# Optimization experiments

Hardware: AMD Instinct MI355X
Metric: run time of the kernel (lower is better)

Reference implementation:

```python
import jax, jax.numpy as jnp
import numpy as np

DIM = 1024
HEADS = 8
HEAD_DIM = DIM // HEADS
TAU = HEAD_DIM ** 0.5
BS, SEQ = 1, 2048


def setup_inputs() -> dict:
    key = jax.random.key(0)
    kq, kk, kv, kb = jax.random.split(key, 4)
    q = jax.random.normal(kq, (BS, SEQ, DIM), jnp.float32)
    k = jax.random.normal(kk, (BS, SEQ, DIM), jnp.float32)
    v = jax.random.normal(kv, (BS, SEQ, DIM), jnp.float32)
    Wi_w = jnp.zeros((HEADS, 3 * DIM), jnp.float32)
    Wi_b = 0.1 * jax.random.normal(kb, (HEADS,), jnp.float32)
    Wf_w = jnp.zeros((HEADS, 3 * DIM), jnp.float32)
    Wf_b = jnp.linspace(3.0, 6.0, HEADS, dtype=jnp.float32)  # equidistant_bias_init(3, 6)
    gn_w = jnp.ones((DIM,), jnp.float32)
    gn_b = jnp.zeros((DIM,), jnp.float32)
    return {"q": q, "k": k, "v": v, "Wi_w": Wi_w, "Wi_b": Wi_b,
            "Wf_w": Wf_w, "Wf_b": Wf_b, "gn_w": gn_w, "gn_b": gn_b}


def reference(q, k, v, Wi_w, Wi_b, Wf_w, Wf_b, gn_w, gn_b):
    bs, seq, dim = q.shape
    gate_in = jnp.concatenate([q, k, v], axis=-1)                    # [b, s, 3d]
    itilde = jnp.einsum('bsd,hd->bhs', gate_in, Wi_w) + Wi_b[None, :, None]
    ftilde = jnp.einsum('bsd,hd->bhs', gate_in, Wf_w) + Wf_b[None, :, None]

    # Decay matrix: F_act[i,j] = sum_{t=j+1..i} logsigmoid(ftilde_t), lower-tri else -inf
    csum = jnp.cumsum(jax.nn.log_sigmoid(ftilde), axis=-1)           # [b, h, s]
    Fmat = csum[..., :, None] - csum[..., None, :]                   # [b, h, s, s]
    mask = jnp.tril(jnp.ones((seq, seq), dtype=bool))
    F_act = jnp.where(mask, Fmat, -jnp.inf)

    Dtilde = F_act + itilde[..., None, :]                            # add input gate along j
    max_d = jnp.max(Dtilde, axis=-1, keepdims=True)
    D = jnp.exp(Dtilde - max_d)                                      # stabilized decay weights

    qh = q.reshape(bs, seq, HEADS, HEAD_DIM).transpose(0, 2, 1, 3)
    kh = k.reshape(bs, seq, HEADS, HEAD_DIM).transpose(0, 2, 1, 3)
    vh = v.reshape(bs, seq, HEADS, HEAD_DIM).transpose(0, 2, 1, 3)

    Ctilde = jnp.einsum('bhid,bhjd->bhij', qh, kh) * D / TAU
    maxit = jnp.maximum(jnp.abs(jnp.sum(Ctilde, axis=-1, keepdims=True)), jnp.exp(-max_d))
    Htilde = jnp.einsum('bhij,bhjd->bhid', Ctilde, vh) / (maxit + 1e-6)

    # GroupNorm(HEADS groups) over dim, applied per token
    x = Htilde.transpose(0, 2, 1, 3).reshape(bs * seq, HEADS, HEAD_DIM)
    mean = jnp.mean(x, axis=-1, keepdims=True)
    var = jnp.var(x, axis=-1, keepdims=True)
    xn = (x - mean) / jnp.sqrt(var + 1e-5)
    out = xn.reshape(bs * seq, DIM) * gn_w + gn_b
    return out.reshape(bs, seq, DIM)
```

## Files before the change

kernel.cpp:

```cpp
#include <hip/hip_runtime.h>
#include <math.h>

#define SEQ 2048
#define NH 8
#define HD 128
#define DIMF 1024
#define LOG2E 1.4426950408889634f
#define INVTAU 0.08838834764831845f

typedef __attribute__((ext_vector_type(8))) short bf16x8;
typedef __attribute__((ext_vector_type(8))) unsigned short us8;
typedef __attribute__((ext_vector_type(4))) float f32x4;
typedef __attribute__((ext_vector_type(16))) float f32x16;

__device__ float g_itacc[NH*SEQ];
__device__ float g_ftacc[NH*SEQ];
__device__ float g_aL[NH*SEQ];
__device__ float g_cmL[NH*SEQ];
__device__ float g_en[NH*SEQ];
__device__ unsigned short g_Qb[NH*SEQ*HD];
__device__ unsigned short g_Kb[NH*SEQ*HD];
__device__ unsigned short g_Vb[NH*SEQ*HD];
__device__ unsigned short g_Vt[NH*HD*SEQ];
__device__ unsigned short g_Wb[16*3072];
__device__ float g_Opart[640*64*128];
__device__ float g_Spart[640*64];

__device__ __forceinline__ unsigned short f2bf(float x) {
  unsigned u = __float_as_uint(x);
  u += 0x7fffu + ((u >> 16) & 1u);
  return (unsigned short)(u >> 16);
}

__device__ __forceinline__ unsigned packbf(float lo, float hi) {
  return (unsigned)f2bf(lo) | ((unsigned)f2bf(hi) << 16);
}

__global__ __launch_bounds__(256) void convert_kernel(const float* __restrict__ q,
                                                      const float* __restrict__ k,
                                                      const float* __restrict__ v,
                                                      const float* __restrict__ Wi,
                                                      const float* __restrict__ Wf) {
  const int bid = blockIdx.x;
  if (bid < 6144) {
    const int s = bid & 2047;
    const int t = bid >> 11;
    const float* src = (t == 0) ? q : (t == 1) ? k : v;
    unsigned short* dst = (t == 0) ? g_Qb : (t == 1) ? g_Kb : g_Vb;
    const int c = threadIdx.x * 4;
    const float4 f = *(const float4*)(src + s*DIMF + c);
    const int h = c >> 7, d = c & 127;
    ushort4 u;
    u.x = f2bf(f.x); u.y = f2bf(f.y); u.z = f2bf(f.z); u.w = f2bf(f.w);
    *(ushort4*)(dst + (h*SEQ + s)*HD + d) = u;
  } else {
    const int gid = (bid - 6144) * 256 + threadIdx.x;
    const int e4 = gid * 4;
    const int p = e4 / 3072;
    const int c = e4 % 3072;
    const float* src = (p < 8) ? (Wi + p*3072 + c) : (Wf + (p-8)*3072 + c);
    const float4 f = *(const float4*)src;
    ushort4 u;
    u.x = f2bf(f.x); u.y = f2bf(f.y); u.z = f2bf(f.z); u.w = f2bf(f.w);
    *(ushort4*)(g_Wb + p*3072 + c) = u;
  }
}

__global__ __launch_bounds__(256) void vtrans_kernel() {
  __shared__ __align__(16) unsigned short Ts[64*72];
  const int h  = blockIdx.x;
  const int s0 = blockIdx.y * 64;
  const int d0 = blockIdx.z * 64;
  const int t = threadIdx.x;
  {
    const int sr = t >> 2;
    const int c  = (t & 3) * 16;
    const unsigned short* src = g_Vb + (h*SEQ + s0 + sr)*HD + d0 + c;
    *(us8*)&Ts[sr*72 + c]     = *(const us8*)&src[0];
    *(us8*)&Ts[sr*72 + c + 8] = *(const us8*)&src[8];
  }
  __syncthreads();
  {
    const int w = t >> 6, l = t & 63;
    unsigned short outv[16];
    #pragma unroll
    for (int j = 0; j < 16; ++j) outv[j] = Ts[(w*16 + j)*72 + l];
    unsigned short* dst = g_Vt + (h*HD + d0 + l)*SEQ + s0 + w*16;
    *(us8*)&dst[0] = *(us8*)&outv[0];
    *(us8*)&dst[8] = *(us8*)&outv[8];
  }
}

__global__ __launch_bounds__(256) void gates_kernel() {
  __shared__ f32x4 red[4][64];
  const int tid = threadIdx.x;
  const int wave = tid >> 6, lane = tid & 63;
  const int q4 = lane >> 4, l16 = lane & 15;
  const int s0 = blockIdx.x * 16;
  f32x4 acc = {0.f, 0.f, 0.f, 0.f};
  #pragma unroll 8
  for (int ks = wave*24; ks < wave*24 + 24; ++ks) {
    const int k0 = ks*32 + q4*8;
    const int tsel = k0 >> 10;
    const int rem = k0 & 1023;
    const int hh = rem >> 7, dd = rem & 127;
    const unsigned short* base = (tsel == 0) ? g_Qb : (tsel == 1) ? g_Kb : g_Vb;
    const bf16x8 a = *(const bf16x8*)&base[(hh*SEQ + s0 + l16)*HD + dd];
    const bf16x8 b = *(const bf16x8*)&g_Wb[l16*3072 + k0];
    acc = __builtin_amdgcn_mfma_f32_16x16x32_bf16(a, b, acc, 0, 0, 0);
  }
  red[wave][lane] = acc;
  __syncthreads();
  if (wave == 0) {
    f32x4 s = red[0][lane];
    #pragma unroll
    for (int w = 1; w < 4; ++w) s += red[w][lane];
    #pragma unroll
    for (int r = 0; r < 4; ++r) {
      const int sg = s0 + 4*q4 + r;
      if (l16 < 8) g_itacc[l16*SEQ + sg] = s[r];
      else         g_ftacc[(l16-8)*SEQ + sg] = s[r];
    }
  }
}

__global__ __launch_bounds__(256) void scan_kernel(const float* __restrict__ Wi_b,
                                                   const float* __restrict__ Wf_b) {
  __shared__ float Wsum[4];
  __shared__ float Wmax[4];
  const int h = blockIdx.x;
  const int t = threadIdx.x;
  const int wave = t >> 6, lane = t & 63;
  const float ib = Wi_b[h];
  const float fb = Wf_b[h];
  const int base = h*SEQ + t*8;

  float it[8], ft[8];
  *(float4*)&it[0] = *(const float4*)&g_itacc[base];
  *(float4*)&it[4] = *(const float4*)&g_itacc[base+4];
  *(float4*)&ft[0] = *(const float4*)&g_ftacc[base];
  *(float4*)&ft[4] = *(const float4*)&g_ftacc[base+4];

  float cs[8];
  float run = 0.f;
  #pragma unroll
  for (int j = 0; j < 8; ++j) {
    const float f = ft[j] + fb;
    const float ls = fminf(f, 0.f) - log1pf(expf(-fabsf(f)));
    run += ls;
    cs[j] = run;
  }
  float x = run;
  #pragma unroll
  for (int off = 1; off < 64; off <<= 1) {
    const float tv = __shfl_up(x, off, 64);
    if (lane >= off) x += tv;
  }
  const float wexcl = x - run;
  if (lane == 63) Wsum[wave] = x;
  __syncthreads();
  float boff = 0.f;
  #pragma unroll
  for (int w = 0; w < 4; ++w) if (w < wave) boff += Wsum[w];
  const float cbase = boff + wexcl;

  float a[8], am[8], csum[8];
  float m = -__builtin_inff();
  #pragma unroll
  for (int j = 0; j < 8; ++j) {
    csum[j] = cbase + cs[j];
    a[j] = (it[j] + ib) - csum[j];
    m = fmaxf(m, a[j]);
    am[j] = m;
  }
  float y = m;
  #pragma unroll
  for (int off = 1; off < 64; off <<= 1) {
    const float tv = __shfl_up(y, off, 64);
    if (lane >= off) y = fmaxf(y, tv);
  }
  float e = __shfl_up(y, 1, 64);
  if (lane == 0) e = -__builtin_inff();
  if (lane == 63) Wmax[wave] = y;
  __syncthreads();
  float bmax = -__builtin_inff();
  #pragma unroll
  for (int w = 0; w < 4; ++w) if (w < wave) bmax = fmaxf(bmax, Wmax[w]);
  const float pre = fmaxf(bmax, e);

  float oa[8], ocm[8], oen[8];
  #pragma unroll
  for (int j = 0; j < 8; ++j) {
    const float cm = fmaxf(pre, am[j]);
    oa[j]  = a[j] * LOG2E;
    ocm[j] = cm * LOG2E;
    oen[j] = expf(-(csum[j] + cm));
  }
  *(float4*)&g_aL[base]    = *(float4*)&oa[0];
  *(float4*)&g_aL[base+4]  = *(float4*)&oa[4];
  *(float4*)&g_cmL[base]   = *(float4*)&ocm[0];
  *(float4*)&g_cmL[base+4] = *(float4*)&ocm[4];
  *(float4*)&g_en[base]    = *(float4*)&oen[0];
  *(float4*)&g_en[base+4]  = *(float4*)&oen[4];
}

__global__ __launch_bounds__(256, 2) void attn1_kernel() {
  __shared__ float Osum[2][32][128];
  __shared__ float Sred[64][2];

  const int y = blockIdx.x;
  const int h = blockIdx.y;
  int g, s0g;
  if      (y < 8)  { g = 0; s0g = 0;  }
  else if (y < 24) { g = 1; s0g = 8;  }
  else if (y < 48) { g = 2; s0g = 24; }
  else             { g = 3; s0g = 48; }
  const int rel = y - s0g;
  const int iT  = 8*g + rel/(g+1);
  const int ch  = rel - (rel/(g+1))*(g+1);
  const int slot = h*80 + y;
  const int i0 = iT*64;
  const int jt0 = ch*8;
  const int jt1 = (jt0 + 8 < iT + 1) ? (jt0 + 8) : (iT + 1);

  const int tid  = threadIdx.x;
  const int wave = tid >> 6;
  const int lane = tid & 63;
  const int l31  = lane & 31;
  const int hi   = lane >> 5;
  const int wr   = wave >> 1;
  const int wc   = wave & 1;

  bf16x8 qf[8];
  {
    const unsigned short* Qg = g_Qb + (h*SEQ + i0 + 32*wr + l31)*HD + hi*8;
    #pragma unroll
    for (int ks = 0; ks < 8; ++ks) qf[ks] = *(const bf16x8*)&Qg[ks*16];
  }
  const float cm = g_cmL[h*SEQ + i0 + 32*wr + l31];
  const int   ig = i0 + 32*wr + l31;

  f32x16 acc[4];
  #pragma unroll
  for (int td = 0; td < 4; ++td)
    #pragma unroll
    for (int e = 0; e < 16; ++e) acc[td][e] = 0.f;
  float rs_sum = 0.f;

  const unsigned short* Kg  = g_Kb + (h*SEQ + 32*wc + l31)*HD + hi*8;
  const unsigned short* Vg  = g_Vt + (h*HD + l31)*SEQ + 32*wc + hi*8;
  const float*          aLg = g_aL + h*SEQ + 32*wc + 4*hi;

  for (int jt = jt0; jt < jt1; ++jt) {
    const int j0 = jt*64;
    bf16x8 kf[8];
    #pragma unroll
    for (int ks = 0; ks < 8; ++ks) kf[ks] = *(const bf16x8*)&Kg[j0*HD + ks*16];
    float4 aLq[4];
    #pragma unroll
    for (int rq = 0; rq < 4; ++rq) aLq[rq] = *(const float4*)&aLg[j0 + 8*rq];

    f32x16 a0, a1;
    #pragma unroll
    for (int e = 0; e < 16; ++e) { a0[e] = 0.f; a1[e] = 0.f; }
    #pragma unroll
    for (int ks = 0; ks < 8; ks += 2) {
      a0 = __builtin_amdgcn_mfma_f32_32x32x16_bf16(kf[ks],   qf[ks],   a0, 0, 0, 0);
      a1 = __builtin_amdgcn_mfma_f32_32x32x16_bf16(kf[ks+1], qf[ks+1], a1, 0, 0, 0);
    }

    const bool diag = (jt == iT);
    const int jbase = j0 + 32*wc + 4*hi;

    #pragma unroll
    for (int ph = 0; ph < 2; ++ph) {
      float pv[8];
      #pragma unroll
      for (int rr = 0; rr < 8; ++rr) {
        const int r  = 8*ph + rr;
        const int rq = r >> 2;
        const float aL = ((const float*)&aLq[rq])[r & 3];
        float p = (a0[r] + a1[r]) * (exp2f(aL - cm) * INVTAU);
        const int jg = jbase + 8*rq + (r & 3);
        if (diag && jg > ig) p = 0.f;
        rs_sum += p;
        pv[rr] = p;
      }
      const unsigned w0 = packbf(pv[0], pv[1]);
      const unsigned w1 = packbf(pv[2], pv[3]);
      const unsigned w2 = packbf(pv[4], pv[5]);
      const unsigned w3 = packbf(pv[6], pv[7]);
      const auto s0 = __builtin_amdgcn_permlane32_swap(w0, w2, false, false);
      const auto s1 = __builtin_amdgcn_permlane32_swap(w1, w3, false, false);
      union { unsigned u[4]; bf16x8 v; } fr;
      fr.u[0] = s0[0]; fr.u[1] = s1[0]; fr.u[2] = s0[1]; fr.u[3] = s1[1];
      #pragma unroll
      for (int td = 0; td < 4; ++td) {
        const bf16x8 vb = *(const bf16x8*)&Vg[(32*td)*SEQ + j0 + 16*ph];
        acc[td] = __builtin_amdgcn_mfma_f32_32x32x16_bf16(fr.v, vb, acc[td], 0, 0, 0);
      }
    }
  }

  rs_sum += __shfl_xor(rs_sum, 32, 64);
  if (hi == 0) Sred[32*wr + l31][wc] = rs_sum;

  if (wc == 0) {
    #pragma unroll
    for (int td = 0; td < 4; ++td)
      #pragma unroll
      for (int r = 0; r < 16; ++r) {
        const int row = (r & 3) + 8*(r >> 2) + 4*hi;
        Osum[wr][row][32*td + l31] = acc[td][r];
      }
  }
  __syncthreads();
  if (wc == 1) {
    float* Ob = g_Opart + slot*(64*128);
    #pragma unroll
    for (int td = 0; td < 4; ++td)
      #pragma unroll
      for (int r = 0; r < 16; ++r) {
        const int row = (r & 3) + 8*(r >> 2) + 4*hi;
        Ob[(32*wr + row)*128 + 32*td + l31] = acc[td][r] + Osum[wr][row][32*td + l31];
      }
  }
  if (tid < 64) g_Spart[slot*64 + tid] = Sred[tid][0] + Sred[tid][1];
}

__global__ __launch_bounds__(256) void reduce_kernel(const float* __restrict__ gnw,
                                                     const float* __restrict__ gnb,
                                                     float* __restrict__ out) {
  const int h  = blockIdx.x;
  const int iT = blockIdx.y;
  const int t  = threadIdx.x;
  const int r  = t >> 2;
  const int qd = t & 3;
  const int qq = iT >> 3;
  const int nch = qq + 1;
  const int slot0 = h*80 + iT + 4*qq*(qq-1) + qq*(iT & 7);

  float acc[32];
  #pragma unroll
  for (int e = 0; e < 32; ++e) acc[e] = 0.f;
  float S = 0.f;
  for (int c = 0; c < nch; ++c) {
    const float* Ob = g_Opart + (slot0 + c)*(64*128) + r*128 + qd*32;
    #pragma unroll
    for (int kk = 0; kk < 8; ++kk) {
      const float4 f = *(const float4*)&Ob[kk*4];
      acc[kk*4+0] += f.x; acc[kk*4+1] += f.y; acc[kk*4+2] += f.z; acc[kk*4+3] += f.w;
    }
    S += g_Spart[(slot0 + c)*64 + r];
  }

  const float en = g_en[h*SEQ + iT*64 + r];
  const float sc = 1.f / (fmaxf(fabsf(S), en) + 1e-6f);
  float s1 = 0.f, s2 = 0.f;
  #pragma unroll
  for (int e = 0; e < 32; ++e) {
    const float xv = acc[e] * sc;
    acc[e] = xv;
    s1 += xv;
    s2 += xv * xv;
  }
  s1 += __shfl_xor(s1, 1, 4); s2 += __shfl_xor(s2, 1, 4);
  s1 += __shfl_xor(s1, 2, 4); s2 += __shfl_xor(s2, 2, 4);
  const float mean = s1 * (1.f/128.f);
  const float var  = s2 * (1.f/128.f) - mean*mean;
  const float rstd = rsqrtf(var + 1e-5f);

  const float* gw = gnw + h*HD + qd*32;
  const float* gb = gnb + h*HD + qd*32;
  float* op = out + (iT*64 + r)*DIMF + h*HD + qd*32;
  #pragma unroll
  for (int kk = 0; kk < 8; ++kk) {
    const float4 w4 = *(const float4*)&gw[kk*4];
    const float4 b4 = *(const float4*)&gb[kk*4];
    float4 o;
    o.x = (acc[kk*4+0] - mean) * rstd * w4.x + b4.x;
    o.y = (acc[kk*4+1] - mean) * rstd * w4.y + b4.y;
    o.z = (acc[kk*4+2] - mean) * rstd * w4.z + b4.z;
    o.w = (acc[kk*4+3] - mean) * rstd * w4.w + b4.w;
    *(float4*)&op[kk*4] = o;
  }
}

extern "C" void kernel_launch(void* const* d_in, const int* in_sizes, int n_in,
                              void* d_out, int out_size, void* d_ws, size_t ws_size,
                              hipStream_t stream) {
  (void)in_sizes; (void)n_in; (void)out_size; (void)d_ws; (void)ws_size;
  const float* q    = (const float*)d_in[0];
  const float* k    = (const float*)d_in[1];
  const float* v    = (const float*)d_in[2];
  const float* Wi_w = (const float*)d_in[3];
  const float* Wi_b = (const float*)d_in[4];
  const float* Wf_w = (const float*)d_in[5];
  const float* Wf_b = (const float*)d_in[6];
  const float* gnw  = (const float*)d_in[7];
  const float* gnb  = (const float*)d_in[8];
  float* out = (float*)d_out;

  convert_kernel<<<dim3(6192), 256, 0, stream>>>(q, k, v, Wi_w, Wf_w);
  vtrans_kernel<<<dim3(NH, SEQ/64, HD/64), 256, 0, stream>>>();
  gates_kernel<<<dim3(128), 256, 0, stream>>>();
  scan_kernel<<<dim3(NH), 256, 0, stream>>>(Wi_b, Wf_b);
  attn1_kernel<<<dim3(80, NH), 256, 0, stream>>>();
  reduce_kernel<<<dim3(NH, SEQ/64), 256, 0, stream>>>(gnw, gnb, out);
}
```

Baseline: 172.9 us.

## Stage K/V tiles in LDS via direct global-to-LDS loads and split work finer

The attention kernel now loads each K and transposed-V 64-row tile into swizzled shared memory with global_load_lds, where all four waves share it. Before, each wave fetched its own fragments straight from global memory. The key-dimension chunks are halved from 8 tiles to 4, so each head gets 144 blocks instead of 80. The grid is reordered so heads vary fastest, and occupancy is raised to 3 blocks per CU. The cost is two barriers per tile with no double buffering, more partial sums for the reduce kernel to combine, and Osum reusing the K/V shared buffer.

```diff
diff --git a/kernel.cpp b/kernel.cpp
--- a/kernel.cpp
+++ b/kernel.cpp
@@ -7,6 +7,7 @@
 #define DIMF 1024
 #define LOG2E 1.4426950408889634f
 #define INVTAU 0.08838834764831845f
+#define NSLOT 144
 
 typedef __attribute__((ext_vector_type(8))) short bf16x8;
 typedef __attribute__((ext_vector_type(8))) unsigned short us8;
@@ -23,8 +24,8 @@
 __device__ unsigned short g_Vb[NH*SEQ*HD];
 __device__ unsigned short g_Vt[NH*HD*SEQ];
 __device__ unsigned short g_Wb[16*3072];
-__device__ float g_Opart[640*64*128];
-__device__ float g_Spart[640*64];
+__device__ float g_Opart[NH*NSLOT*64*128];
+__device__ float g_Spart[NH*NSLOT*64];
 
 __device__ __forceinline__ unsigned short f2bf(float x) {
   unsigned u = __float_as_uint(x);
@@ -34,6 +35,12 @@
 
 __device__ __forceinline__ unsigned packbf(float lo, float hi) {
   return (unsigned)f2bf(lo) | ((unsigned)f2bf(hi) << 16);
+}
+
+__device__ __forceinline__ void gload16(const unsigned short* g, unsigned short* l) {
+  __builtin_amdgcn_global_load_lds(
+      (const __attribute__((address_space(1))) unsigned int*)g,
+      (__attribute__((address_space(3))) unsigned int*)l, 16, 0, 0);
 }
 
 __global__ __launch_bounds__(256) void convert_kernel(const float* __restrict__ q,
@@ -204,24 +211,24 @@
   *(float4*)&g_en[base+4]  = *(float4*)&oen[4];
 }
 
-__global__ __launch_bounds__(256, 2) void attn1_kernel() {
-  __shared__ float Osum[2][32][128];
-  __shared__ float Sred[64][2];
-
-  const int y = blockIdx.x;
-  const int h = blockIdx.y;
-  int g, s0g;
-  if      (y < 8)  { g = 0; s0g = 0;  }
-  else if (y < 24) { g = 1; s0g = 8;  }
-  else if (y < 48) { g = 2; s0g = 24; }
-  else             { g = 3; s0g = 48; }
+__global__ __launch_bounds__(256, 3) void attn1_kernel() {
+  __shared__ __align__(16) unsigned char smem[33280];
+  unsigned short* Ks = (unsigned short*)smem;
+  unsigned short* Vt = (unsigned short*)(smem + 16384);
+  float (*Osum)[32][128] = (float (*)[32][128])smem;
+  float (*Sred)[2] = (float (*)[2])(smem + 32768);
+
+  const int h = blockIdx.x;
+  const int y = blockIdx.y;
+  int q = 0, s0g = 0;
+  while (y >= s0g + 4*(q+1)) { s0g += 4*(q+1); ++q; }
   const int rel = y - s0g;
-  const int iT  = 8*g + rel/(g+1);
-  const int ch  = rel - (rel/(g+1))*(g+1);
-  const int slot = h*80 + y;
+  const int iT  = 4*q + rel/(q+1);
+  const int ch  = rel - (rel/(q+1))*(q+1);
+  const int slot = h*NSLOT + y;
   const int i0 = iT*64;
-  const int jt0 = ch*8;
-  const int jt1 = (jt0 + 8 < iT + 1) ? (jt0 + 8) : (iT + 1);
+  const int jt0 = ch*4;
+  const int jt1 = (jt0 + 4 < iT + 1) ? (jt0 + 4) : (iT + 1);
 
   const int tid  = threadIdx.x;
   const int wave = tid >> 6;
@@ -230,6 +237,7 @@
   const int hi   = lane >> 5;
   const int wr   = wave >> 1;
   const int wc   = wave & 1;
+  const int wbase = __builtin_amdgcn_readfirstlane(wave);
 
   bf16x8 qf[8];
   {
@@ -247,26 +255,49 @@
     for (int e = 0; e < 16; ++e) acc[td][e] = 0.f;
   float rs_sum = 0.f;
 
-  const unsigned short* Kg  = g_Kb + (h*SEQ + 32*wc + l31)*HD + hi*8;
-  const unsigned short* Vg  = g_Vt + (h*HD + l31)*SEQ + 32*wc + hi*8;
+  const unsigned short* Kgh = g_Kb + h*SEQ*HD;
+  const unsigned short* Vgh = g_Vt + h*HD*SEQ;
   const float*          aLg = g_aL + h*SEQ + 32*wc + 4*hi;
+
+  int pK[4], pV[4];
+  #pragma unroll
+  for (int gi = 0; gi < 4; ++gi) {
+    const int s  = (wave*4 + gi)*64 + lane;
+    const int rK = s >> 4;
+    const int cK = (s & 15) ^ (rK & 15);
+    pK[gi] = rK*HD + cK*8;
+    const int dV = s >> 3;
+    const int cV = (s & 7) ^ (dV & 7);
+    pV[gi] = dV*SEQ + cV*8;
+  }
+
+  const int rI = 32*wc + l31;
+  const unsigned short* KsRow = &Ks[rI*128];
+  const int swK = rI & 15;
 
   for (int jt = jt0; jt < jt1; ++jt) {
     const int j0 = jt*64;
-    bf16x8 kf[8];
-    #pragma unroll
-    for (int ks = 0; ks < 8; ++ks) kf[ks] = *(const bf16x8*)&Kg[j0*HD + ks*16];
+    __syncthreads();
+    #pragma unroll
+    for (int gi = 0; gi < 4; ++gi) {
+      gload16(Kgh + j0*HD + pK[gi], &Ks[(wbase*4 + gi)*512]);
+      gload16(Vgh + j0     + pV[gi], &Vt[(wbase*4 + gi)*512]);
+    }
     float4 aLq[4];
     #pragma unroll
     for (int rq = 0; rq < 4; ++rq) aLq[rq] = *(const float4*)&aLg[j0 + 8*rq];
+    asm volatile("s_waitcnt vmcnt(0)" ::: "memory");
+    __syncthreads();
 
     f32x16 a0, a1;
     #pragma unroll
     for (int e = 0; e < 16; ++e) { a0[e] = 0.f; a1[e] = 0.f; }
     #pragma unroll
     for (int ks = 0; ks < 8; ks += 2) {
-      a0 = __builtin_amdgcn_mfma_f32_32x32x16_bf16(kf[ks],   qf[ks],   a0, 0, 0, 0);
-      a1 = __builtin_amdgcn_mfma_f32_32x32x16_bf16(kf[ks+1], qf[ks+1], a1, 0, 0, 0);
+      const bf16x8 k0v = *(const bf16x8*)&KsRow[((ks*2 + hi)     ^ swK)*8];
+      const bf16x8 k1v = *(const bf16x8*)&KsRow[(((ks+1)*2 + hi) ^ swK)*8];
+      a0 = __builtin_amdgcn_mfma_f32_32x32x16_bf16(k0v, qf[ks],   a0, 0, 0, 0);
+      a1 = __builtin_amdgcn_mfma_f32_32x32x16_bf16(k1v, qf[ks+1], a1, 0, 0, 0);
     }
 
     const bool diag = (jt == iT);
@@ -296,7 +327,8 @@
       fr.u[0] = s0[0]; fr.u[1] = s1[0]; fr.u[2] = s0[1]; fr.u[3] = s1[1];
       #pragma unroll
       for (int td = 0; td < 4; ++td) {
-        const bf16x8 vb = *(const bf16x8*)&Vg[(32*td)*SEQ + j0 + 16*ph];
+        const int d = 32*td + l31;
+        const bf16x8 vb = *(const bf16x8*)&Vt[d*64 + (((4*wc + 2*ph + hi) ^ (d & 7))*8)];
         acc[td] = __builtin_amdgcn_mfma_f32_32x32x16_bf16(fr.v, vb, acc[td], 0, 0, 0);
       }
     }
@@ -304,6 +336,7 @@
 
   rs_sum += __shfl_xor(rs_sum, 32, 64);
   if (hi == 0) Sred[32*wr + l31][wc] = rs_sum;
+  __syncthreads();
 
   if (wc == 0) {
     #pragma unroll
@@ -336,9 +369,9 @@
   const int t  = threadIdx.x;
   const int r  = t >> 2;
   const int qd = t & 3;
-  const int qq = iT >> 3;
+  const int qq = iT >> 2;
   const int nch = qq + 1;
-  const int slot0 = h*80 + iT + 4*qq*(qq-1) + qq*(iT & 7);
+  const int slot0 = h*NSLOT + 2*qq*(qq+1) + (iT & 3)*(qq + 1);
 
   float acc[32];
   #pragma unroll
@@ -405,6 +438,6 @@
   vtrans_kernel<<<dim3(NH, SEQ/64, HD/64), 256, 0, stream>>>();
   gates_kernel<<<dim3(128), 256, 0, stream>>>();
   scan_kernel<<<dim3(NH), 256, 0, stream>>>(Wi_b, Wf_b);
-  attn1_kernel<<<dim3(80, NH), 256, 0, stream>>>();
+  attn1_kernel<<<dim3(NH, NSLOT), 256, 0, stream>>>();
   reduce_kernel<<<dim3(NH, SEQ/64), 256, 0, stream>>>(gnw, gnb, out);
 }
```

After: 168.5 us. 1.03x faster.

## Fuse attention and GroupNorm reduction with paired causal tiles per block

Applied to the files above, without the earlier changes.

Replaces the split-K attention kernel and its separate reduce kernel with one kernel. Each block pairs a short and a long 32-row query tile (y and 63-y) so the causal work is balanced, shares the K/V loads between both tiles, and double-buffers K/V in registers. The partial sums are reduced in shared memory and the GroupNorm epilogue runs in the same kernel. This removes the partial-output round trip through global memory and one launch. In exchange the grid is smaller (256 blocks at one block per CU) and register pressure is high.

```diff
diff --git a/kernel.cpp b/kernel.cpp
--- a/kernel.cpp
+++ b/kernel.cpp
@@ -23,8 +23,6 @@
 __device__ unsigned short g_Vb[NH*SEQ*HD];
 __device__ unsigned short g_Vt[NH*HD*SEQ];
 __device__ unsigned short g_Wb[16*3072];
-__device__ float g_Opart[640*64*128];
-__device__ float g_Spart[640*64];
 
 __device__ __forceinline__ unsigned short f2bf(float x) {
   unsigned u = __float_as_uint(x);
@@ -204,186 +202,198 @@
   *(float4*)&g_en[base+4]  = *(float4*)&oen[4];
 }
 
-__global__ __launch_bounds__(256, 2) void attn1_kernel() {
-  __shared__ float Osum[2][32][128];
-  __shared__ float Sred[64][2];
-
-  const int y = blockIdx.x;
-  const int h = blockIdx.y;
-  int g, s0g;
-  if      (y < 8)  { g = 0; s0g = 0;  }
-  else if (y < 24) { g = 1; s0g = 8;  }
-  else if (y < 48) { g = 2; s0g = 24; }
-  else             { g = 3; s0g = 48; }
-  const int rel = y - s0g;
-  const int iT  = 8*g + rel/(g+1);
-  const int ch  = rel - (rel/(g+1))*(g+1);
-  const int slot = h*80 + y;
-  const int i0 = iT*64;
-  const int jt0 = ch*8;
-  const int jt1 = (jt0 + 8 < iT + 1) ? (jt0 + 8) : (iT + 1);
+__global__ __launch_bounds__(256, 1) void attn_kernel(const float* __restrict__ gnw,
+                                                      const float* __restrict__ gnb,
+                                                      float* __restrict__ out) {
+  __shared__ float Osum[2][32][132];
+  __shared__ float Sred[4][32];
+
+  const int h = blockIdx.x;
+  const int y = blockIdx.y;
+  const int tS = y, tB = 63 - y;
+  const int iS0 = 32*tS, iB0 = 32*tB;
+  const int iSmax = iS0 + 31, iBmax = iB0 + 31;
+  const int nvB = tB/4 + 1;
 
   const int tid  = threadIdx.x;
-  const int wave = tid >> 6;
+  const int w    = tid >> 6;
   const int lane = tid & 63;
   const int l31  = lane & 31;
   const int hi   = lane >> 5;
-  const int wr   = wave >> 1;
-  const int wc   = wave & 1;
-
-  bf16x8 qf[8];
+
+  const unsigned short* Kgh = g_Kb + (h*SEQ + l31)*HD + hi*8;
+  const unsigned short* Vgh = g_Vt + (h*HD + l31)*SEQ + hi*8;
+  const float*          aLh = g_aL + h*SEQ + 4*hi;
+
+  bf16x8 qfS[8], qfB[8];
   {
-    const unsigned short* Qg = g_Qb + (h*SEQ + i0 + 32*wr + l31)*HD + hi*8;
-    #pragma unroll
-    for (int ks = 0; ks < 8; ++ks) qf[ks] = *(const bf16x8*)&Qg[ks*16];
-  }
-  const float cm = g_cmL[h*SEQ + i0 + 32*wr + l31];
-  const int   ig = i0 + 32*wr + l31;
-
-  f32x16 acc[4];
+    const unsigned short* QS = g_Qb + (h*SEQ + iS0 + l31)*HD + hi*8;
+    const unsigned short* QB = g_Qb + (h*SEQ + iB0 + l31)*HD + hi*8;
+    #pragma unroll
+    for (int ks = 0; ks < 8; ++ks) {
+      qfS[ks] = *(const bf16x8*)&QS[ks*16];
+      qfB[ks] = *(const bf16x8*)&QB[ks*16];
+    }
+  }
+  const float cmS = g_cmL[h*SEQ + iS0 + l31];
+  const float cmB = g_cmL[h*SEQ + iB0 + l31];
+  const int   igS = iS0 + l31, igB = iB0 + l31;
+
+  f32x16 accS[4], accB[4];
   #pragma unroll
   for (int td = 0; td < 4; ++td)
     #pragma unroll
-    for (int e = 0; e < 16; ++e) acc[td][e] = 0.f;
-  float rs_sum = 0.f;
-
-  const unsigned short* Kg  = g_Kb + (h*SEQ + 32*wc + l31)*HD + hi*8;
-  const unsigned short* Vg  = g_Vt + (h*HD + l31)*SEQ + 32*wc + hi*8;
-  const float*          aLg = g_aL + h*SEQ + 32*wc + 4*hi;
-
-  for (int jt = jt0; jt < jt1; ++jt) {
-    const int j0 = jt*64;
-    bf16x8 kf[8];
-    #pragma unroll
-    for (int ks = 0; ks < 8; ++ks) kf[ks] = *(const bf16x8*)&Kg[j0*HD + ks*16];
-    float4 aLq[4];
-    #pragma unroll
-    for (int rq = 0; rq < 4; ++rq) aLq[rq] = *(const float4*)&aLg[j0 + 8*rq];
-
-    f32x16 a0, a1;
-    #pragma unroll
-    for (int e = 0; e < 16; ++e) { a0[e] = 0.f; a1[e] = 0.f; }
+    for (int e = 0; e < 16; ++e) { accS[td][e] = 0.f; accB[td][e] = 0.f; }
+  float rsS = 0.f, rsB = 0.f;
+
+  bf16x8 Ka[8], Va[8], Kb[8], Vb[8];
+
+  auto LOAD = [&](bf16x8 (&K)[8], bf16x8 (&V)[8], int jc) {
+    const int jw = jc*128 + 32*w;
+    #pragma unroll
+    for (int ks = 0; ks < 8; ++ks)
+      K[ks] = *(const bf16x8*)&Kgh[jw*HD + ks*16];
+    #pragma unroll
+    for (int td = 0; td < 4; ++td)
+      #pragma unroll
+      for (int ph = 0; ph < 2; ++ph)
+        V[td*2 + ph] = *(const bf16x8*)&Vgh[(32*td)*SEQ + jw + 16*ph];
+  };
+
+  auto TILE = [&](int jw, const bf16x8 (&K)[8], const bf16x8 (&V)[8],
+                  const float4 (&aLq)[4], const bf16x8 (&qf)[8],
+                  float cm, int ig, int i0t, f32x16 (&acc)[4], float& rsum) {
+    f32x16 s0a, s1a;
+    #pragma unroll
+    for (int e = 0; e < 16; ++e) { s0a[e] = 0.f; s1a[e] = 0.f; }
     #pragma unroll
     for (int ks = 0; ks < 8; ks += 2) {
-      a0 = __builtin_amdgcn_mfma_f32_32x32x16_bf16(kf[ks],   qf[ks],   a0, 0, 0, 0);
-      a1 = __builtin_amdgcn_mfma_f32_32x32x16_bf16(kf[ks+1], qf[ks+1], a1, 0, 0, 0);
-    }
-
-    const bool diag = (jt == iT);
-    const int jbase = j0 + 32*wc + 4*hi;
-
+      s0a = __builtin_amdgcn_mfma_f32_32x32x16_bf16(K[ks],   qf[ks],   s0a, 0, 0, 0);
+      s1a = __builtin_amdgcn_mfma_f32_32x32x16_bf16(K[ks+1], qf[ks+1], s1a, 0, 0, 0);
+    }
+    const bool needMask = (jw + 31 > i0t);
     #pragma unroll
     for (int ph = 0; ph < 2; ++ph) {
       float pv[8];
-      #pragma unroll
-      for (int rr = 0; rr < 8; ++rr) {
-        const int r  = 8*ph + rr;
-        const int rq = r >> 2;
-        const float aL = ((const float*)&aLq[rq])[r & 3];
-        float p = (a0[r] + a1[r]) * (exp2f(aL - cm) * INVTAU);
-        const int jg = jbase + 8*rq + (r & 3);
-        if (diag && jg > ig) p = 0.f;
-        rs_sum += p;
-        pv[rr] = p;
+      if (needMask) {
+        #pragma unroll
+        for (int rr = 0; rr < 8; ++rr) {
+          const int r  = 8*ph + rr;
+          const int rq = r >> 2;
+          const float aL = ((const float*)&aLq[rq])[r & 3];
+          float p = (s0a[r] + s1a[r]) * (exp2f(aL - cm) * INVTAU);
+          const int jg = jw + 8*rq + 4*hi + (r & 3);
+          if (jg > ig) p = 0.f;
+          rsum += p;
+          pv[rr] = p;
+        }
+      } else {
+        #pragma unroll
+        for (int rr = 0; rr < 8; ++rr) {
+          const int r  = 8*ph + rr;
+          const int rq = r >> 2;
+          const float aL = ((const float*)&aLq[rq])[r & 3];
+          const float p = (s0a[r] + s1a[r]) * (exp2f(aL - cm) * INVTAU);
+          rsum += p;
+          pv[rr] = p;
+        }
       }
       const unsigned w0 = packbf(pv[0], pv[1]);
       const unsigned w1 = packbf(pv[2], pv[3]);
       const unsigned w2 = packbf(pv[4], pv[5]);
       const unsigned w3 = packbf(pv[6], pv[7]);
-      const auto s0 = __builtin_amdgcn_permlane32_swap(w0, w2, false, false);
-      const auto s1 = __builtin_amdgcn_permlane32_swap(w1, w3, false, false);
+      const auto p0 = __builtin_amdgcn_permlane32_swap(w0, w2, false, false);
+      const auto p1 = __builtin_amdgcn_permlane32_swap(w1, w3, false, false);
       union { unsigned u[4]; bf16x8 v; } fr;
-      fr.u[0] = s0[0]; fr.u[1] = s1[0]; fr.u[2] = s0[1]; fr.u[3] = s1[1];
+      fr.u[0] = p0[0]; fr.u[1] = p1[0]; fr.u[2] = p0[1]; fr.u[3] = p1[1];
       #pragma unroll
-      for (int td = 0; td < 4; ++td) {
-        const bf16x8 vb = *(const bf16x8*)&Vg[(32*td)*SEQ + j0 + 16*ph];
-        acc[td] = __builtin_amdgcn_mfma_f32_32x32x16_bf16(fr.v, vb, acc[td], 0, 0, 0);
-      }
-    }
-  }
-
-  rs_sum += __shfl_xor(rs_sum, 32, 64);
-  if (hi == 0) Sred[32*wr + l31][wc] = rs_sum;
-
-  if (wc == 0) {
-    #pragma unroll
-    for (int td = 0; td < 4; ++td)
+      for (int td = 0; td < 4; ++td)
+        acc[td] = __builtin_amdgcn_mfma_f32_32x32x16_bf16(fr.v, V[td*2 + ph], acc[td], 0, 0, 0);
+    }
+  };
+
+  auto STEP = [&](int jc, const bf16x8 (&K)[8], const bf16x8 (&V)[8]) {
+    const int jw = jc*128 + 32*w;
+    float4 aLq[4];
+    #pragma unroll
+    for (int rq = 0; rq < 4; ++rq) aLq[rq] = *(const float4*)&aLh[jw + 8*rq];
+    if (jw <= iBmax) TILE(jw, K, V, aLq, qfB, cmB, igB, iB0, accB, rsB);
+    if (jw <= iSmax) TILE(jw, K, V, aLq, qfS, cmS, igS, iS0, accS, rsS);
+  };
+
+  LOAD(Ka, Va, 0);
+  int jc = 0;
+  for (; jc + 2 <= nvB; jc += 2) {
+    LOAD(Kb, Vb, jc + 1);
+    STEP(jc, Ka, Va);
+    if (jc + 2 < nvB) LOAD(Ka, Va, jc + 2);
+    STEP(jc + 1, Kb, Vb);
+  }
+  if (jc < nvB) STEP(jc, Ka, Va);
+
+  const float* gw = gnw + h*HD;
+  const float* gb = gnb + h*HD;
+  auto EPI = [&](f32x16 (&acc)[4], float rsum, int i0t) {
+    const float rs2 = rsum + __shfl_xor(rsum, 32, 64);
+    if (hi == 0) Sred[w][l31] = rs2;
+    if (w >= 2) {
       #pragma unroll
-      for (int r = 0; r < 16; ++r) {
-        const int row = (r & 3) + 8*(r >> 2) + 4*hi;
-        Osum[wr][row][32*td + l31] = acc[td][r];
-      }
-  }
+      for (int td = 0; td < 4; ++td)
+        #pragma unroll
+        for (int r = 0; r < 16; ++r) {
+          const int row = (r & 3) + 8*(r >> 2) + 4*hi;
+          Osum[w - 2][row][32*td + l31] = acc[td][r];
+        }
+    }
+    __syncthreads();
+    if (w < 2) {
+      #pragma unroll
+      for (int td = 0; td < 4; ++td)
+        #pragma unroll
+        for (int r = 0; r < 16; ++r) {
+          const int row = (r & 3) + 8*(r >> 2) + 4*hi;
+          Osum[w][row][32*td + l31] += acc[td][r];
+        }
+    }
+    __syncthreads();
+    const int i  = tid >> 3;
+    const int d0 = (tid & 7) * 16;
+    float o[16];
+    #pragma unroll
+    for (int e = 0; e < 16; e += 4) {
+      const float4 a0 = *(const float4*)&Osum[0][i][d0 + e];
+      const float4 a1 = *(const float4*)&Osum[1][i][d0 + e];
+      o[e+0] = a0.x + a1.x; o[e+1] = a0.y + a1.y;
+      o[e+2] = a0.z + a1.z; o[e+3] = a0.w + a1.w;
+    }
+    const float S  = Sred[0][i] + Sred[1][i] + Sred[2][i] + Sred[3][i];
+    const float en = g_en[h*SEQ + i0t + i];
+    const float sc = 1.f / (fmaxf(fabsf(S), en) + 1e-6f);
+    float s1 = 0.f, s2 = 0.f;
+    #pragma unroll
+    for (int e = 0; e < 16; ++e) { const float xv = o[e]*sc; o[e] = xv; s1 += xv; s2 += xv*xv; }
+    #pragma unroll
+    for (int m = 1; m < 8; m <<= 1) { s1 += __shfl_xor(s1, m, 8); s2 += __shfl_xor(s2, m, 8); }
+    const float mean = s1 * (1.f/128.f);
+    const float var  = s2 * (1.f/128.f) - mean*mean;
+    const float rstd = rsqrtf(var + 1e-5f);
+    float* op = out + (i0t + i)*DIMF + h*HD + d0;
+    #pragma unroll
+    for (int e = 0; e < 16; e += 4) {
+      const float4 w4 = *(const float4*)&gw[d0 + e];
+      const float4 b4 = *(const float4*)&gb[d0 + e];
+      float4 ov;
+      ov.x = (o[e+0] - mean) * rstd * w4.x + b4.x;
+      ov.y = (o[e+1] - mean) * rstd * w4.y + b4.y;
+      ov.z = (o[e+2] - mean) * rstd * w4.z + b4.z;
+      ov.w = (o[e+3] - mean) * rstd * w4.w + b4.w;
+      *(float4*)&op[e] = ov;
+    }
+  };
+
+  EPI(accS, rsS, iS0);
   __syncthreads();
-  if (wc == 1) {
-    float* Ob = g_Opart + slot*(64*128);
-    #pragma unroll
-    for (int td = 0; td < 4; ++td)
-      #pragma unroll
-      for (int r = 0; r < 16; ++r) {
-        const int row = (r & 3) + 8*(r >> 2) + 4*hi;
-        Ob[(32*wr + row)*128 + 32*td + l31] = acc[td][r] + Osum[wr][row][32*td + l31];
-      }
-  }
-  if (tid < 64) g_Spart[slot*64 + tid] = Sred[tid][0] + Sred[tid][1];
-}
-
-__global__ __launch_bounds__(256) void reduce_kernel(const float* __restrict__ gnw,
-                                                     const float* __restrict__ gnb,
-                                                     float* __restrict__ out) {
-  const int h  = blockIdx.x;
-  const int iT = blockIdx.y;
-  const int t  = threadIdx.x;
-  const int r  = t >> 2;
-  const int qd = t & 3;
-  const int qq = iT >> 3;
-  const int nch = qq + 1;
-  const int slot0 = h*80 + iT + 4*qq*(qq-1) + qq*(iT & 7);
-
-  float acc[32];
-  #pragma unroll
-  for (int e = 0; e < 32; ++e) acc[e] = 0.f;
-  float S = 0.f;
-  for (int c = 0; c < nch; ++c) {
-    const float* Ob = g_Opart + (slot0 + c)*(64*128) + r*128 + qd*32;
-    #pragma unroll
-    for (int kk = 0; kk < 8; ++kk) {
-      const float4 f = *(const float4*)&Ob[kk*4];
-      acc[kk*4+0] += f.x; acc[kk*4+1] += f.y; acc[kk*4+2] += f.z; acc[kk*4+3] += f.w;
-    }
-    S += g_Spart[(slot0 + c)*64 + r];
-  }
-
-  const float en = g_en[h*SEQ + iT*64 + r];
-  const float sc = 1.f / (fmaxf(fabsf(S), en) + 1e-6f);
-  float s1 = 0.f, s2 = 0.f;
-  #pragma unroll
-  for (int e = 0; e < 32; ++e) {
-    const float xv = acc[e] * sc;
-    acc[e] = xv;
-    s1 += xv;
-    s2 += xv * xv;
-  }
-  s1 += __shfl_xor(s1, 1, 4); s2 += __shfl_xor(s2, 1, 4);
-  s1 += __shfl_xor(s1, 2, 4); s2 += __shfl_xor(s2, 2, 4);
-  const float mean = s1 * (1.f/128.f);
-  const float var  = s2 * (1.f/128.f) - mean*mean;
-  const float rstd = rsqrtf(var + 1e-5f);
-
-  const float* gw = gnw + h*HD + qd*32;
-  const float* gb = gnb + h*HD + qd*32;
-  float* op = out + (iT*64 + r)*DIMF + h*HD + qd*32;
-  #pragma unroll
-  for (int kk = 0; kk < 8; ++kk) {
-    const float4 w4 = *(const float4*)&gw[kk*4];
-    const float4 b4 = *(const float4*)&gb[kk*4];
-    float4 o;
-    o.x = (acc[kk*4+0] - mean) * rstd * w4.x + b4.x;
-    o.y = (acc[kk*4+1] - mean) * rstd * w4.y + b4.y;
-    o.z = (acc[kk*4+2] - mean) * rstd * w4.z + b4.z;
-    o.w = (acc[kk*4+3] - mean) * rstd * w4.w + b4.w;
-    *(float4*)&op[kk*4] = o;
-  }
+  EPI(accB, rsB, iB0);
 }
 
 extern "C" void kernel_launch(void* const* d_in, const int* in_sizes, int n_in,
@@ -405,6 +415,5 @@
   vtrans_kernel<<<dim3(NH, SEQ/64, HD/64), 256, 0, stream>>>();
   gates_kernel<<<dim3(128), 256, 0, stream>>>();
   scan_kernel<<<dim3(NH), 256, 0, stream>>>(Wi_b, Wf_b);
-  attn1_kernel<<<dim3(80, NH), 256, 0, stream>>>();
-  reduce_kernel<<<dim3(NH, SEQ/64), 256, 0, stream>>>(gnw, gnb, out);
-}
+  attn_kernel<<<dim3(NH, 32), 256, 0, stream>>>(gnw, gnb, out);
+}
```

After: 145.8 us. -15.7%, faster.
